# Optimization experiments

Hardware: AMD Instinct MI355X
Metric: run time of the kernel (lower is better)

The kernel has to match this reference:

```python
import jax, jax.numpy as jnp
import numpy as np

HD = 64          # head_dim
PX = 32          # patches_x
PY = 32          # patches_y
IW = 512.0       # image_width
IH = 512.0       # image_height
C = 4            # cameras
B = 1
H = 12
S = C * PX * PY  # 4096


def _rope_coeffs(pos, feat_dim):
    nf = feat_dim // 2
    freqs = 100.0 ** (-jnp.arange(nf, dtype=jnp.float32) / nf)  # freq_base=100, freq_scale=1
    ang = pos[:, None].astype(jnp.float32) * freqs[None, :]
    # broadcast shape (1, seqlen, 1, nf)
    return jnp.cos(ang)[None, :, None, :], jnp.sin(ang)[None, :, None, :]


def _rope(x, cs, inverse=False):
    cos, sin = cs
    h = x.shape[-1] // 2
    xi, yi = x[..., :h], x[..., h:]
    if inverse:
        return jnp.concatenate([cos * xi - sin * yi, sin * xi + cos * yi], -1)
    return jnp.concatenate([cos * xi + sin * yi, -sin * xi + cos * yi], -1)


def _proj(x, M):
    # x: (b, s, n, f), M: (b, c, D, D) per-camera projection applied to D-sized sub-blocks
    b, s, n, f = x.shape
    c, D = M.shape[1], M.shape[-1]
    xr = x.reshape(b, c, s // c, n, f // D, D)
    return jnp.einsum('bcij,bcpnkj->bcpnki', M, xr).reshape(b, s, n, f)


def _invert_SE3(T):
    Rinv = jnp.swapaxes(T[..., :3, :3], -1, -2)
    t = -jnp.einsum('...ij,...j->...i', Rinv, T[..., :3, 3])
    top = jnp.concatenate([Rinv, t[..., None]], -1)            # (..., 3, 4)
    bot = jnp.zeros_like(top[..., :1, :]).at[..., 0, 3].set(1.0)
    return jnp.concatenate([top, bot], -2)


def _lift_K(K):
    out = jnp.zeros(K.shape[:-2] + (4, 4), K.dtype)
    return out.at[..., :3, :3].set(K).at[..., 3, 3].set(1.0)


def _invert_K(K):
    out = jnp.zeros_like(K)
    out = out.at[..., 0, 0].set(1.0 / K[..., 0, 0]).at[..., 1, 1].set(1.0 / K[..., 1, 1])
    out = out.at[..., 0, 2].set(-K[..., 0, 2] / K[..., 0, 0]).at[..., 1, 2].set(-K[..., 1, 2] / K[..., 1, 1])
    return out.at[..., 2, 2].set(1.0)


def setup_inputs() -> dict:
    key = jax.random.key(0)
    kq, kk, kv, kr, kt, kf = jax.random.split(key, 6)
    q = jax.random.normal(kq, (B, S, H, HD), dtype=jnp.float32)
    k = jax.random.normal(kk, (B, S, H, HD), dtype=jnp.float32)
    v = jax.random.normal(kv, (B, S, H, HD), dtype=jnp.float32)
    # proper SE(3) viewmats: random rotations (det +1) + translations
    A = jax.random.normal(kr, (B, C, 3, 3), dtype=jnp.float32)
    Q, _ = jnp.linalg.qr(A)
    Q = Q * jnp.sign(jnp.linalg.det(Q))[..., None, None]  # det(sQ)=s^3 det(Q) for 3x3
    t = jax.random.normal(kt, (B, C, 3, 1), dtype=jnp.float32)
    top = jnp.concatenate([Q, t], -1)
    bot = jnp.tile(jnp.array([0.0, 0.0, 0.0, 1.0], jnp.float32)[None, None, None, :], (B, C, 1, 1))
    viewmats = jnp.concatenate([top, bot], -2)
    # realistic pinhole intrinsics
    f = 400.0 + 200.0 * jax.random.uniform(kf, (B, C, 2), dtype=jnp.float32)
    Ks = jnp.zeros((B, C, 3, 3), jnp.float32)
    Ks = Ks.at[..., 0, 0].set(f[..., 0]).at[..., 1, 1].set(f[..., 1])
    Ks = Ks.at[..., 0, 2].set(IW / 2).at[..., 1, 2].set(IH / 2).at[..., 2, 2].set(1.0)
    return {'q': q, 'k': k, 'v': v, 'viewmats': viewmats, 'Ks': Ks}


def reference(q, k, v, viewmats, Ks):
    # normalize intrinsics to [-0.5, 0.5] image coords
    Ksn = jnp.zeros_like(Ks)
    Ksn = Ksn.at[..., 0, 0].set(Ks[..., 0, 0] / IW).at[..., 1, 1].set(Ks[..., 1, 1] / IH)
    Ksn = Ksn.at[..., 0, 2].set(Ks[..., 0, 2] / IW - 0.5).at[..., 1, 2].set(Ks[..., 1, 2] / IH - 0.5)
    Ksn = Ksn.at[..., 2, 2].set(1.0)
    P = jnp.einsum('...ij,...jk->...ik', _lift_K(Ksn), viewmats)         # (B,C,4,4)
    P_T = jnp.swapaxes(P, -1, -2)
    P_inv = jnp.einsum('...ij,...jk->...ik', _invert_SE3(viewmats), _lift_K(_invert_K(Ksn)))
    # 2-D patch positions, tiled over cameras (num_register_tokens=0)
    pos_x = jnp.tile(jnp.arange(PX), (PY * C,))
    pos_y = jnp.tile(jnp.repeat(jnp.arange(PY), PX), (C,))
    cx = _rope_coeffs(pos_x, HD // 4)
    cy = _rope_coeffs(pos_y, HD // 4)
    h2, h4 = HD // 2, HD // 4

    def tq(x):
        return jnp.concatenate([_proj(x[..., :h2], P_T), _rope(x[..., h2:h2 + h4], cx), _rope(x[..., h2 + h4:], cy)], -1)

    def tkv(x):
        return jnp.concatenate([_proj(x[..., :h2], P_inv), _rope(x[..., h2:h2 + h4], cx), _rope(x[..., h2 + h4:], cy)], -1)

    def to(x):
        return jnp.concatenate([_proj(x[..., :h2], P), _rope(x[..., h2:h2 + h4], cx, True), _rope(x[..., h2 + h4:], cy, True)], -1)

    qh, kh, vh = tq(q), tkv(k), tkv(v)
    scale = 1.0 / jnp.sqrt(jnp.float32(HD))
    scores = jnp.einsum('bqhd,bkhd->bhqk', qh, kh) * scale
    w = jax.nn.softmax(scores, axis=-1)
    out = jnp.einsum('bhqk,bkhd->bqhd', w, vh)
    return to(out)
```

## Files before the change

kernel.cpp:

```cpp
#include <hip/hip_runtime.h>
#include <cstdint>

#define SQ 4096
#define NH 12
#define NC 4
#define KVB 64
#define NT (SQ / KVB)

typedef __attribute__((ext_vector_type(8))) __bf16 bf16x8;
typedef __attribute__((ext_vector_type(8))) short short8;
typedef __attribute__((ext_vector_type(4))) short s16x4;
typedef __attribute__((ext_vector_type(4))) float f32x4;
typedef __attribute__((ext_vector_type(16))) float f32x16;
typedef __attribute__((ext_vector_type(4))) unsigned int u32x4;
typedef __attribute__((ext_vector_type(2))) unsigned int u32x2;

__device__ __forceinline__ unsigned short f2bf(float f) {
  unsigned int u = __float_as_uint(f);
  u += 0x7FFFu + ((u >> 16) & 1u);
  return (unsigned short)(u >> 16);
}

__device__ __forceinline__ unsigned int cvtpk(float lo, float hi) {
  unsigned int r;
  asm("v_cvt_pk_bf16_f32 %0, %1, %2" : "=v"(r) : "v"(lo), "v"(hi));
  return r;
}

__global__ void prep_kernel(const float* __restrict__ viewmats, const float* __restrict__ Ks,
                            float* __restrict__ mats, float* __restrict__ ct, float* __restrict__ st) {
  int t = threadIdx.x;
  int pos = t >> 3, jf = t & 7;
  float fr = powf(100.0f, -(float)jf / 8.0f);
  float ang = (float)pos * fr;
  ct[t] = cosf(ang);
  st[t] = sinf(ang);
  if (t < NC) {
    const float* V = viewmats + t * 16;
    const float* K = Ks + t * 9;
    float fx = K[0] * (1.0f / 512.0f);
    float fy = K[4] * (1.0f / 512.0f);
    float cx = K[2] * (1.0f / 512.0f) - 0.5f;
    float cy = K[5] * (1.0f / 512.0f) - 0.5f;
    float P[16], PT[16], IV[16], PI[16];
    for (int jj = 0; jj < 4; jj++) {
      P[0 * 4 + jj] = fx * V[0 * 4 + jj] + cx * V[2 * 4 + jj];
      P[1 * 4 + jj] = fy * V[1 * 4 + jj] + cy * V[2 * 4 + jj];
      P[2 * 4 + jj] = V[2 * 4 + jj];
      P[3 * 4 + jj] = V[3 * 4 + jj];
    }
    for (int i = 0; i < 4; i++)
      for (int jj = 0; jj < 4; jj++) PT[i * 4 + jj] = P[jj * 4 + i];
    for (int i = 0; i < 3; i++) {
      for (int jj = 0; jj < 3; jj++) IV[i * 4 + jj] = V[jj * 4 + i];
      IV[i * 4 + 3] = -(V[3] * V[0 * 4 + i] + V[7] * V[1 * 4 + i] + V[11] * V[2 * 4 + i]);
    }
    IV[12] = 0.f; IV[13] = 0.f; IV[14] = 0.f; IV[15] = 1.f;
    float rfx = 1.0f / fx, rfy = 1.0f / fy;
    for (int i = 0; i < 4; i++) {
      PI[i * 4 + 0] = IV[i * 4 + 0] * rfx;
      PI[i * 4 + 1] = IV[i * 4 + 1] * rfy;
      PI[i * 4 + 2] = -cx * rfx * IV[i * 4 + 0] - cy * rfy * IV[i * 4 + 1] + IV[i * 4 + 2];
      PI[i * 4 + 3] = IV[i * 4 + 3];
    }
    for (int ii = 0; ii < 16; ii++) {
      mats[0   + t * 16 + ii] = PT[ii];
      mats[64  + t * 16 + ii] = PI[ii];
      mats[128 + t * 16 + ii] = P[ii];
    }
  }
}

__device__ __forceinline__ float4 tr_row(float4 x, int j, int s, const float* __restrict__ M,
                                         const float* __restrict__ ct, const float* __restrict__ st,
                                         bool inv) {
  float px = __shfl_xor(x.x, 2);
  float py = __shfl_xor(x.y, 2);
  float pz = __shfl_xor(x.z, 2);
  float pw = __shfl_xor(x.w, 2);
  float4 y;
  if (j < 8) {
    y.x = M[0] * x.x + M[1] * x.y + M[2]  * x.z + M[3]  * x.w;
    y.y = M[4] * x.x + M[5] * x.y + M[6]  * x.z + M[7]  * x.w;
    y.z = M[8] * x.x + M[9] * x.y + M[10] * x.z + M[11] * x.w;
    y.w = M[12] * x.x + M[13] * x.y + M[14] * x.z + M[15] * x.w;
  } else {
    bool isx = (((j >> 1) & 1) == 0);
    int pos = (j < 12) ? (s & 31) : ((s >> 5) & 31);
    float sgn = isx ? 1.0f : -1.0f;
    if (inv) sgn = -sgn;
    int fb = (4 * j) & 7;
    const float* c = ct + pos * 8 + fb;
    const float* sn = st + pos * 8 + fb;
    y.x = c[0] * x.x + sgn * sn[0] * px;
    y.y = c[1] * x.y + sgn * sn[1] * py;
    y.z = c[2] * x.z + sgn * sn[2] * pz;
    y.w = c[3] * x.w + sgn * sn[3] * pw;
  }
  return y;
}

__device__ __forceinline__ void store_bf4(unsigned short* p, float4 v) {
  s16x4 r;
  r[0] = (short)f2bf(v.x); r[1] = (short)f2bf(v.y);
  r[2] = (short)f2bf(v.z); r[3] = (short)f2bf(v.w);
  *(s16x4*)p = r;
}

__global__ __launch_bounds__(256) void transform_kernel(
    const float* __restrict__ q, const float* __restrict__ k, const float* __restrict__ v,
    const float* __restrict__ mats, const float* __restrict__ ct, const float* __restrict__ st,
    unsigned short* __restrict__ qh, unsigned short* __restrict__ kh, unsigned short* __restrict__ vh) {
  const int t = threadIdx.x;
  const int lane = t & 63, w = t >> 6;
  const int row = blockIdx.x * 16 + w * 4 + (lane >> 4);
  const int j = lane & 15;
  const int s = row / NH;
  const int h = row - s * NH;
  const int cam = s >> 10;
  const size_t ioff = (size_t)row * 64 + j * 4;
  const size_t ooff = (size_t)h * (SQ * 64) + (size_t)s * 64 + j * 4;
  float4 xq = *(const float4*)(q + ioff);
  float4 xk = *(const float4*)(k + ioff);
  float4 xv = *(const float4*)(v + ioff);
  float4 yq = tr_row(xq, j, s, mats + cam * 16, ct, st, false);
  float4 yk = tr_row(xk, j, s, mats + 64 + cam * 16, ct, st, false);
  float4 yv = tr_row(xv, j, s, mats + 64 + cam * 16, ct, st, false);
  const float SC = 0.1803368801111204f;
  yq.x *= SC; yq.y *= SC; yq.z *= SC; yq.w *= SC;
  store_bf4(qh + ooff, yq);
  store_bf4(kh + ooff, yk);
  store_bf4(vh + ooff, yv);
}

__global__ __launch_bounds__(128) void attn_kernel(const unsigned short* __restrict__ qh,
                                                   const unsigned short* __restrict__ kh,
                                                   const unsigned short* __restrict__ vh,
                                                   float* __restrict__ oh) {
  __shared__ __align__(16) short Kl[2][KVB * 64];
  __shared__ __align__(16) short Vl[2][KVB * 64];
  const int t = threadIdx.x;
  const int lane = t & 63;
  const int w = t >> 6;
  const int hi = lane >> 5;
  const int l31 = lane & 31;
  const int sw7 = l31 & 7;
  const int h = blockIdx.y;
  const int q0 = blockIdx.x * 64 + w * 32;
  const size_t hbase = (size_t)h * SQ * 64;

  bf16x8 qf[4];
  {
    const unsigned short* qp = qh + hbase + (size_t)(q0 + l31) * 64 + hi * 8;
#pragma unroll
    for (int ds = 0; ds < 4; ++ds) qf[ds] = *(const bf16x8*)(qp + ds * 16);
  }

  int kr[4], kg[4], kidx[4];
#pragma unroll
  for (int i = 0; i < 4; ++i) {
    int c = t + 128 * i;
    kr[i] = c >> 3;
    kg[i] = c & 7;
    kidx[i] = kr[i] * 64 + ((kg[i] ^ (kr[i] & 7)) << 3);
  }
  const int va = t & 15;
  const int vD0 = (t >> 4) * 8;

  float m = -1e30f, l = 0.f;
  f32x16 oac0, oac1;
#pragma unroll
  for (int r = 0; r < 16; ++r) { oac0[r] = 0.f; oac1[r] = 0.f; }

  short8 kst[4], vst[4];

  auto issue_loads = [&](int kt) {
#pragma unroll
    for (int i = 0; i < 4; ++i)
      kst[i] = *(const short8*)(kh + hbase + (size_t)(kt + kr[i]) * 64 + kg[i] * 8);
    const unsigned short* vp = vh + hbase + (size_t)(kt + 4 * va) * 64 + vD0;
#pragma unroll
    for (int i = 0; i < 4; ++i) vst[i] = *(const short8*)(vp + i * 64);
  };

  auto write_lds = [&](int buf) {
    short* K = Kl[buf];
#pragma unroll
    for (int i = 0; i < 4; ++i) *(short8*)(K + kidx[i]) = kst[i];
    short* V = Vl[buf];
#pragma unroll
    for (int dd = 0; dd < 8; ++dd) {
      int d = vD0 + dd;
      unsigned int w0 = (unsigned int)(unsigned short)vst[0][dd] |
                        ((unsigned int)(unsigned short)vst[1][dd] << 16);
      unsigned int w1 = (unsigned int)(unsigned short)vst[2][dd] |
                        ((unsigned int)(unsigned short)vst[3][dd] << 16);
      u32x2 pk; pk[0] = w0; pk[1] = w1;
      int idx = d * 64 + ((((va >> 1)) ^ (d & 7)) << 3) + (va & 1) * 4;
      *(u32x2*)(V + idx) = pk;
    }
  };

  issue_loads(0);
  write_lds(0);
  __syncthreads();

#define MKFRAG(sv, base, out)                                          \
  {                                                                    \
    unsigned int a0 = cvtpk(sv[base + 0], sv[base + 1]);               \
    unsigned int b0 = cvtpk(sv[base + 4], sv[base + 5]);               \
    asm volatile("v_permlane32_swap_b32 %0, %1" : "+v"(a0), "+v"(b0)); \
    unsigned int a1 = cvtpk(sv[base + 2], sv[base + 3]);               \
    unsigned int b1 = cvtpk(sv[base + 6], sv[base + 7]);               \
    asm volatile("v_permlane32_swap_b32 %0, %1" : "+v"(a1), "+v"(b1)); \
    u32x4 u; u[0] = a0; u[1] = a1; u[2] = b0; u[3] = b1;               \
    out = __builtin_bit_cast(bf16x8, u);                               \
  }

  for (int it = 0; it < NT; ++it) {
    const int cur = it & 1;
    const bool pf = (it + 1 < NT);
    if (pf) issue_loads((it + 1) * KVB);

    const short* K = Kl[cur];
    const short* V = Vl[cur];

    f32x16 s0, s1;
#pragma unroll
    for (int r = 0; r < 16; ++r) { s0[r] = 0.f; s1[r] = 0.f; }
#pragma unroll
    for (int ds = 0; ds < 4; ++ds) {
      bf16x8 k0 = *(const bf16x8*)(K + (0 * 32 + l31) * 64 + (((hi + 2 * ds) ^ sw7) << 3));
      bf16x8 k1 = *(const bf16x8*)(K + (1 * 32 + l31) * 64 + (((hi + 2 * ds) ^ sw7) << 3));
      s0 = __builtin_amdgcn_mfma_f32_32x32x16_bf16(k0, qf[ds], s0, 0, 0, 0);
      s1 = __builtin_amdgcn_mfma_f32_32x32x16_bf16(k1, qf[ds], s1, 0, 0, 0);
    }

    float pm = s0[0];
#pragma unroll
    for (int r = 1; r < 16; ++r) pm = fmaxf(pm, s0[r]);
#pragma unroll
    for (int r = 0; r < 16; ++r) pm = fmaxf(pm, s1[r]);
    pm = fmaxf(pm, __shfl_xor(pm, 32));
    if (!__all(pm - m <= 8.0f)) {
      float mn = fmaxf(m, pm);
      float al = __builtin_amdgcn_exp2f(m - mn);
      m = mn;
      l *= al;
#pragma unroll
      for (int r = 0; r < 16; ++r) {
        int qrow = (r & 3) + 8 * (r >> 2) + 4 * hi;
        float av = __shfl(al, qrow);
        oac0[r] *= av;
        oac1[r] *= av;
      }
    }
    float rs = 0.f;
#pragma unroll
    for (int r = 0; r < 16; ++r) { s0[r] = __builtin_amdgcn_exp2f(s0[r] - m); rs += s0[r]; }
#pragma unroll
    for (int r = 0; r < 16; ++r) { s1[r] = __builtin_amdgcn_exp2f(s1[r] - m); rs += s1[r]; }
    rs += __shfl_xor(rs, 32);
    l += rs;

    bf16x8 pa00, pa01, pa10, pa11;
    MKFRAG(s0, 0, pa00);
    MKFRAG(s0, 8, pa01);
    MKFRAG(s1, 0, pa10);
    MKFRAG(s1, 8, pa11);

    if (pf) write_lds(cur ^ 1);

#pragma unroll
    for (int db = 0; db < 2; ++db) {
      const int rb = (db * 32 + l31) * 64;
      bf16x8 v00 = *(const bf16x8*)(V + rb + (((0 + hi) ^ sw7) << 3));
      bf16x8 v01 = *(const bf16x8*)(V + rb + (((2 + hi) ^ sw7) << 3));
      bf16x8 v10 = *(const bf16x8*)(V + rb + (((4 + hi) ^ sw7) << 3));
      bf16x8 v11 = *(const bf16x8*)(V + rb + (((6 + hi) ^ sw7) << 3));
      if (db == 0) {
        oac0 = __builtin_amdgcn_mfma_f32_32x32x16_bf16(pa00, v00, oac0, 0, 0, 0);
        oac0 = __builtin_amdgcn_mfma_f32_32x32x16_bf16(pa01, v01, oac0, 0, 0, 0);
        oac0 = __builtin_amdgcn_mfma_f32_32x32x16_bf16(pa10, v10, oac0, 0, 0, 0);
        oac0 = __builtin_amdgcn_mfma_f32_32x32x16_bf16(pa11, v11, oac0, 0, 0, 0);
      } else {
        oac1 = __builtin_amdgcn_mfma_f32_32x32x16_bf16(pa00, v00, oac1, 0, 0, 0);
        oac1 = __builtin_amdgcn_mfma_f32_32x32x16_bf16(pa01, v01, oac1, 0, 0, 0);
        oac1 = __builtin_amdgcn_mfma_f32_32x32x16_bf16(pa10, v10, oac1, 0, 0, 0);
        oac1 = __builtin_amdgcn_mfma_f32_32x32x16_bf16(pa11, v11, oac1, 0, 0, 0);
      }
    }
    __syncthreads();
  }

  float linv = 1.0f / l;
  float* op = oh + hbase;
#pragma unroll
  for (int r = 0; r < 16; ++r) {
    int qrow = (r & 3) + 8 * (r >> 2) + 4 * hi;
    float lv = __shfl(linv, qrow);
    op[(size_t)(q0 + qrow) * 64 + l31] = oac0[r] * lv;
    op[(size_t)(q0 + qrow) * 64 + 32 + l31] = oac1[r] * lv;
  }
}

__global__ __launch_bounds__(256) void outtr_kernel(const float* __restrict__ oh,
                                                    const float* __restrict__ mats,
                                                    const float* __restrict__ ct,
                                                    const float* __restrict__ st,
                                                    float* __restrict__ out) {
  const int t = threadIdx.x;
  const int lane = t & 63, w = t >> 6;
  const int row = blockIdx.x * 16 + w * 4 + (lane >> 4);
  const int j = lane & 15;
  const int s = row / NH;
  const int h = row - s * NH;
  const int cam = s >> 10;
  float4 x = *(const float4*)(oh + (size_t)h * (SQ * 64) + (size_t)s * 64 + j * 4);
  float4 y = tr_row(x, j, s, mats + 128 + cam * 16, ct, st, true);
  *(float4*)(out + (size_t)row * 64 + j * 4) = y;
}

extern "C" void kernel_launch(void* const* d_in, const int* in_sizes, int n_in,
                              void* d_out, int out_size, void* d_ws, size_t ws_size,
                              hipStream_t stream) {
  const float* q = (const float*)d_in[0];
  const float* k = (const float*)d_in[1];
  const float* v = (const float*)d_in[2];
  const float* vm = (const float*)d_in[3];
  const float* Ks = (const float*)d_in[4];

  char* ws = (char*)d_ws;
  float* mats = (float*)ws;
  float* ct = (float*)(ws + 1024);
  float* st = (float*)(ws + 2048);
  unsigned short* qh = (unsigned short*)(ws + 4096);
  unsigned short* kh = qh + (size_t)NH * SQ * 64;
  unsigned short* vh = kh + (size_t)NH * SQ * 64;
  float* oh = (float*)(ws + 4096 + 3ull * NH * SQ * 64 * 2);

  hipLaunchKernelGGL(prep_kernel, dim3(1), dim3(256), 0, stream, vm, Ks, mats, ct, st);
  hipLaunchKernelGGL(transform_kernel, dim3((SQ * NH) / 16), dim3(256), 0, stream,
                     q, k, v, mats, ct, st, qh, kh, vh);
  hipLaunchKernelGGL(attn_kernel, dim3(SQ / 64, NH), dim3(128), 0, stream, qh, kh, vh, oh);
  hipLaunchKernelGGL(outtr_kernel, dim3((SQ * NH) / 16), dim3(256), 0, stream,
                     oh, mats, ct, st, (float*)d_out);
}
```

Before: 204.7 us.

## Split attention KV range across two blocks and merge partials in output transform

The attention kernel now splits the key/value sequence into two halves along a new grid dimension, doubling the block count from 768 to 1536 to fill the GPU's compute units. Each half writes bf16 partial outputs plus per-row max and sum, and the output transform kernel merges the two halves with log-sum-exp weights before applying the inverse projection and RoPE. The LDS double buffer becomes a single buffer with an extra barrier, and launch bounds request 3 blocks per unit. Transform code is also restructured into per-branch helpers with vectorized matrix and cos/sin loads. The extra partial-output traffic and the bf16 rounding of partials are the costs.

```diff
diff --git a/kernel.cpp b/kernel.cpp
--- a/kernel.cpp
+++ b/kernel.cpp
@@ -5,7 +5,8 @@
 #define NH 12
 #define NC 4
 #define KVB 64
-#define NT (SQ / KVB)
+#define NSPLIT 2
+#define NTS (SQ / NSPLIT / KVB)
 
 typedef __attribute__((ext_vector_type(8))) __bf16 bf16x8;
 typedef __attribute__((ext_vector_type(8))) short short8;
@@ -20,7 +21,9 @@
   u += 0x7FFFu + ((u >> 16) & 1u);
   return (unsigned short)(u >> 16);
 }
-
+__device__ __forceinline__ float bf2f(unsigned short u) {
+  return __uint_as_float(((unsigned int)u) << 16);
+}
 __device__ __forceinline__ unsigned int cvtpk(float lo, float hi) {
   unsigned int r;
   asm("v_cvt_pk_bf16_f32 %0, %1, %2" : "=v"(r) : "v"(lo), "v"(hi));
@@ -71,35 +74,28 @@
   }
 }
 
-__device__ __forceinline__ float4 tr_row(float4 x, int j, int s, const float* __restrict__ M,
-                                         const float* __restrict__ ct, const float* __restrict__ st,
-                                         bool inv) {
-  float px = __shfl_xor(x.x, 2);
-  float py = __shfl_xor(x.y, 2);
-  float pz = __shfl_xor(x.z, 2);
-  float pw = __shfl_xor(x.w, 2);
+__device__ __forceinline__ float4 mat4(const float4 M[4], float4 x) {
   float4 y;
-  if (j < 8) {
-    y.x = M[0] * x.x + M[1] * x.y + M[2]  * x.z + M[3]  * x.w;
-    y.y = M[4] * x.x + M[5] * x.y + M[6]  * x.z + M[7]  * x.w;
-    y.z = M[8] * x.x + M[9] * x.y + M[10] * x.z + M[11] * x.w;
-    y.w = M[12] * x.x + M[13] * x.y + M[14] * x.z + M[15] * x.w;
-  } else {
-    bool isx = (((j >> 1) & 1) == 0);
-    int pos = (j < 12) ? (s & 31) : ((s >> 5) & 31);
-    float sgn = isx ? 1.0f : -1.0f;
-    if (inv) sgn = -sgn;
-    int fb = (4 * j) & 7;
-    const float* c = ct + pos * 8 + fb;
-    const float* sn = st + pos * 8 + fb;
-    y.x = c[0] * x.x + sgn * sn[0] * px;
-    y.y = c[1] * x.y + sgn * sn[1] * py;
-    y.z = c[2] * x.z + sgn * sn[2] * pz;
-    y.w = c[3] * x.w + sgn * sn[3] * pw;
-  }
+  y.x = M[0].x * x.x + M[0].y * x.y + M[0].z * x.z + M[0].w * x.w;
+  y.y = M[1].x * x.x + M[1].y * x.y + M[1].z * x.z + M[1].w * x.w;
+  y.z = M[2].x * x.x + M[2].y * x.y + M[2].z * x.z + M[2].w * x.w;
+  y.w = M[3].x * x.x + M[3].y * x.y + M[3].z * x.z + M[3].w * x.w;
   return y;
 }
-
+__device__ __forceinline__ float4 rope4(float4 x, float4 p, float4 c, float4 sn, float sgn) {
+  float4 y;
+  y.x = c.x * x.x + sgn * sn.x * p.x;
+  y.y = c.y * x.y + sgn * sn.y * p.y;
+  y.z = c.z * x.z + sgn * sn.z * p.z;
+  y.w = c.w * x.w + sgn * sn.w * p.w;
+  return y;
+}
+__device__ __forceinline__ float4 sxor2(float4 x) {
+  float4 p;
+  p.x = __shfl_xor(x.x, 2); p.y = __shfl_xor(x.y, 2);
+  p.z = __shfl_xor(x.z, 2); p.w = __shfl_xor(x.w, 2);
+  return p;
+}
 __device__ __forceinline__ void store_bf4(unsigned short* p, float4 v) {
   s16x4 r;
   r[0] = (short)f2bf(v.x); r[1] = (short)f2bf(v.y);
@@ -123,9 +119,26 @@
   float4 xq = *(const float4*)(q + ioff);
   float4 xk = *(const float4*)(k + ioff);
   float4 xv = *(const float4*)(v + ioff);
-  float4 yq = tr_row(xq, j, s, mats + cam * 16, ct, st, false);
-  float4 yk = tr_row(xk, j, s, mats + 64 + cam * 16, ct, st, false);
-  float4 yv = tr_row(xv, j, s, mats + 64 + cam * 16, ct, st, false);
+  float4 pq = sxor2(xq), pk = sxor2(xk), pv = sxor2(xv);
+  float4 yq, yk, yv;
+  if (j < 8) {
+    float4 Mq[4], Mk[4];
+    const float4* mq = (const float4*)(mats + cam * 16);
+    const float4* mk = (const float4*)(mats + 64 + cam * 16);
+#pragma unroll
+    for (int i = 0; i < 4; ++i) { Mq[i] = mq[i]; Mk[i] = mk[i]; }
+    yq = mat4(Mq, xq); yk = mat4(Mk, xk); yv = mat4(Mk, xv);
+  } else {
+    bool isx = (((j >> 1) & 1) == 0);
+    int pos = (j < 12) ? (s & 31) : ((s >> 5) & 31);
+    float sgn = isx ? 1.0f : -1.0f;
+    int fb = (j & 1) * 4;
+    float4 c = *(const float4*)(ct + pos * 8 + fb);
+    float4 sn = *(const float4*)(st + pos * 8 + fb);
+    yq = rope4(xq, pq, c, sn, sgn);
+    yk = rope4(xk, pk, c, sn, sgn);
+    yv = rope4(xv, pv, c, sn, sgn);
+  }
   const float SC = 0.1803368801111204f;
   yq.x *= SC; yq.y *= SC; yq.z *= SC; yq.w *= SC;
   store_bf4(qh + ooff, yq);
@@ -133,12 +146,13 @@
   store_bf4(vh + ooff, yv);
 }
 
-__global__ __launch_bounds__(128) void attn_kernel(const unsigned short* __restrict__ qh,
-                                                   const unsigned short* __restrict__ kh,
-                                                   const unsigned short* __restrict__ vh,
-                                                   float* __restrict__ oh) {
-  __shared__ __align__(16) short Kl[2][KVB * 64];
-  __shared__ __align__(16) short Vl[2][KVB * 64];
+__global__ __launch_bounds__(128, 3) void attn_kernel(const unsigned short* __restrict__ qh,
+                                                      const unsigned short* __restrict__ kh,
+                                                      const unsigned short* __restrict__ vh,
+                                                      unsigned short* __restrict__ opart,
+                                                      float2* __restrict__ mlbuf) {
+  __shared__ __align__(16) short Kl[KVB * 64];
+  __shared__ __align__(16) short Vl[KVB * 64];
   const int t = threadIdx.x;
   const int lane = t & 63;
   const int w = t >> 6;
@@ -146,7 +160,9 @@
   const int l31 = lane & 31;
   const int sw7 = l31 & 7;
   const int h = blockIdx.y;
+  const int sp = blockIdx.z;
   const int q0 = blockIdx.x * 64 + w * 32;
+  const int kbase = sp * (SQ / NSPLIT);
   const size_t hbase = (size_t)h * SQ * 64;
 
   bf16x8 qf[4];
@@ -183,11 +199,9 @@
     for (int i = 0; i < 4; ++i) vst[i] = *(const short8*)(vp + i * 64);
   };
 
-  auto write_lds = [&](int buf) {
-    short* K = Kl[buf];
-#pragma unroll
-    for (int i = 0; i < 4; ++i) *(short8*)(K + kidx[i]) = kst[i];
-    short* V = Vl[buf];
+  auto write_lds = [&]() {
+#pragma unroll
+    for (int i = 0; i < 4; ++i) *(short8*)(Kl + kidx[i]) = kst[i];
 #pragma unroll
     for (int dd = 0; dd < 8; ++dd) {
       int d = vD0 + dd;
@@ -197,12 +211,12 @@
                         ((unsigned int)(unsigned short)vst[3][dd] << 16);
       u32x2 pk; pk[0] = w0; pk[1] = w1;
       int idx = d * 64 + ((((va >> 1)) ^ (d & 7)) << 3) + (va & 1) * 4;
-      *(u32x2*)(V + idx) = pk;
+      *(u32x2*)(Vl + idx) = pk;
     }
   };
 
-  issue_loads(0);
-  write_lds(0);
+  issue_loads(kbase);
+  write_lds();
   __syncthreads();
 
 #define MKFRAG(sv, base, out)                                          \
@@ -217,21 +231,17 @@
     out = __builtin_bit_cast(bf16x8, u);                               \
   }
 
-  for (int it = 0; it < NT; ++it) {
-    const int cur = it & 1;
-    const bool pf = (it + 1 < NT);
-    if (pf) issue_loads((it + 1) * KVB);
-
-    const short* K = Kl[cur];
-    const short* V = Vl[cur];
+  for (int it = 0; it < NTS; ++it) {
+    const bool pf = (it + 1 < NTS);
+    if (pf) issue_loads(kbase + (it + 1) * KVB);
 
     f32x16 s0, s1;
 #pragma unroll
     for (int r = 0; r < 16; ++r) { s0[r] = 0.f; s1[r] = 0.f; }
 #pragma unroll
     for (int ds = 0; ds < 4; ++ds) {
-      bf16x8 k0 = *(const bf16x8*)(K + (0 * 32 + l31) * 64 + (((hi + 2 * ds) ^ sw7) << 3));
-      bf16x8 k1 = *(const bf16x8*)(K + (1 * 32 + l31) * 64 + (((hi + 2 * ds) ^ sw7) << 3));
+      bf16x8 k0 = *(const bf16x8*)(Kl + (0 * 32 + l31) * 64 + (((hi + 2 * ds) ^ sw7) << 3));
+      bf16x8 k1 = *(const bf16x8*)(Kl + (1 * 32 + l31) * 64 + (((hi + 2 * ds) ^ sw7) << 3));
       s0 = __builtin_amdgcn_mfma_f32_32x32x16_bf16(k0, qf[ds], s0, 0, 0, 0);
       s1 = __builtin_amdgcn_mfma_f32_32x32x16_bf16(k1, qf[ds], s1, 0, 0, 0);
     }
@@ -269,15 +279,13 @@
     MKFRAG(s1, 0, pa10);
     MKFRAG(s1, 8, pa11);
 
-    if (pf) write_lds(cur ^ 1);
-
 #pragma unroll
     for (int db = 0; db < 2; ++db) {
       const int rb = (db * 32 + l31) * 64;
-      bf16x8 v00 = *(const bf16x8*)(V + rb + (((0 + hi) ^ sw7) << 3));
-      bf16x8 v01 = *(const bf16x8*)(V + rb + (((2 + hi) ^ sw7) << 3));
-      bf16x8 v10 = *(const bf16x8*)(V + rb + (((4 + hi) ^ sw7) << 3));
-      bf16x8 v11 = *(const bf16x8*)(V + rb + (((6 + hi) ^ sw7) << 3));
+      bf16x8 v00 = *(const bf16x8*)(Vl + rb + (((0 + hi) ^ sw7) << 3));
+      bf16x8 v01 = *(const bf16x8*)(Vl + rb + (((2 + hi) ^ sw7) << 3));
+      bf16x8 v10 = *(const bf16x8*)(Vl + rb + (((4 + hi) ^ sw7) << 3));
+      bf16x8 v11 = *(const bf16x8*)(Vl + rb + (((6 + hi) ^ sw7) << 3));
       if (db == 0) {
         oac0 = __builtin_amdgcn_mfma_f32_32x32x16_bf16(pa00, v00, oac0, 0, 0, 0);
         oac0 = __builtin_amdgcn_mfma_f32_32x32x16_bf16(pa01, v01, oac0, 0, 0, 0);
@@ -291,20 +299,26 @@
       }
     }
     __syncthreads();
+    if (pf) {
+      write_lds();
+      __syncthreads();
+    }
   }
 
   float linv = 1.0f / l;
-  float* op = oh + hbase;
+  unsigned short* op = opart + (size_t)sp * NH * SQ * 64 + hbase;
 #pragma unroll
   for (int r = 0; r < 16; ++r) {
     int qrow = (r & 3) + 8 * (r >> 2) + 4 * hi;
     float lv = __shfl(linv, qrow);
-    op[(size_t)(q0 + qrow) * 64 + l31] = oac0[r] * lv;
-    op[(size_t)(q0 + qrow) * 64 + 32 + l31] = oac1[r] * lv;
-  }
-}
-
-__global__ __launch_bounds__(256) void outtr_kernel(const float* __restrict__ oh,
+    op[(size_t)(q0 + qrow) * 64 + l31] = f2bf(oac0[r] * lv);
+    op[(size_t)(q0 + qrow) * 64 + 32 + l31] = f2bf(oac1[r] * lv);
+  }
+  if (hi == 0) mlbuf[(size_t)sp * NH * SQ + (size_t)h * SQ + q0 + l31] = make_float2(m, l);
+}
+
+__global__ __launch_bounds__(256) void outtr_kernel(const unsigned short* __restrict__ opart,
+                                                    const float2* __restrict__ mlbuf,
                                                     const float* __restrict__ mats,
                                                     const float* __restrict__ ct,
                                                     const float* __restrict__ st,
@@ -316,8 +330,41 @@
   const int s = row / NH;
   const int h = row - s * NH;
   const int cam = s >> 10;
-  float4 x = *(const float4*)(oh + (size_t)h * (SQ * 64) + (size_t)s * 64 + j * 4);
-  float4 y = tr_row(x, j, s, mats + 128 + cam * 16, ct, st, true);
+
+  float2 a = mlbuf[(size_t)h * SQ + s];
+  float2 b = mlbuf[(size_t)NH * SQ + (size_t)h * SQ + s];
+  float m = fmaxf(a.x, b.x);
+  float w1 = __builtin_amdgcn_exp2f(a.x - m) * a.y;
+  float w2 = __builtin_amdgcn_exp2f(b.x - m) * b.y;
+  float inv = 1.0f / (w1 + w2);
+  w1 *= inv; w2 *= inv;
+
+  const size_t po = (size_t)h * (SQ * 64) + (size_t)s * 64 + j * 4;
+  s16x4 r1 = *(const s16x4*)(opart + po);
+  s16x4 r2 = *(const s16x4*)(opart + (size_t)NH * SQ * 64 + po);
+  float4 x;
+  x.x = bf2f((unsigned short)r1[0]) * w1 + bf2f((unsigned short)r2[0]) * w2;
+  x.y = bf2f((unsigned short)r1[1]) * w1 + bf2f((unsigned short)r2[1]) * w2;
+  x.z = bf2f((unsigned short)r1[2]) * w1 + bf2f((unsigned short)r2[2]) * w2;
+  x.w = bf2f((unsigned short)r1[3]) * w1 + bf2f((unsigned short)r2[3]) * w2;
+
+  float4 p = sxor2(x);
+  float4 y;
+  if (j < 8) {
+    float4 M[4];
+    const float4* mp = (const float4*)(mats + 128 + cam * 16);
+#pragma unroll
+    for (int i = 0; i < 4; ++i) M[i] = mp[i];
+    y = mat4(M, x);
+  } else {
+    bool isx = (((j >> 1) & 1) == 0);
+    int pos = (j < 12) ? (s & 31) : ((s >> 5) & 31);
+    float sgn = isx ? -1.0f : 1.0f;
+    int fb = (j & 1) * 4;
+    float4 c = *(const float4*)(ct + pos * 8 + fb);
+    float4 sn = *(const float4*)(st + pos * 8 + fb);
+    y = rope4(x, p, c, sn, sgn);
+  }
   *(float4*)(out + (size_t)row * 64 + j * 4) = y;
 }
 
@@ -334,15 +381,18 @@
   float* mats = (float*)ws;
   float* ct = (float*)(ws + 1024);
   float* st = (float*)(ws + 2048);
+  const size_t HSZ = (size_t)NH * SQ * 64;
   unsigned short* qh = (unsigned short*)(ws + 4096);
-  unsigned short* kh = qh + (size_t)NH * SQ * 64;
-  unsigned short* vh = kh + (size_t)NH * SQ * 64;
-  float* oh = (float*)(ws + 4096 + 3ull * NH * SQ * 64 * 2);
+  unsigned short* kh = qh + HSZ;
+  unsigned short* vh = kh + HSZ;
+  unsigned short* opart = vh + HSZ;
+  float2* mlbuf = (float2*)(opart + (size_t)NSPLIT * HSZ);
 
   hipLaunchKernelGGL(prep_kernel, dim3(1), dim3(256), 0, stream, vm, Ks, mats, ct, st);
   hipLaunchKernelGGL(transform_kernel, dim3((SQ * NH) / 16), dim3(256), 0, stream,
                      q, k, v, mats, ct, st, qh, kh, vh);
-  hipLaunchKernelGGL(attn_kernel, dim3(SQ / 64, NH), dim3(128), 0, stream, qh, kh, vh, oh);
+  hipLaunchKernelGGL(attn_kernel, dim3(SQ / 64, NH, NSPLIT), dim3(128), 0, stream,
+                     qh, kh, vh, opart, mlbuf);
   hipLaunchKernelGGL(outtr_kernel, dim3((SQ * NH) / 16), dim3(256), 0, stream,
-                     oh, mats, ct, st, (float*)d_out);
-}
+                     opart, mlbuf, mats, ct, st, (float*)d_out);
+}
```

Result: faster. 188.2 us (-8.0%).
